# Optimization experiments

Hardware: AMD Instinct MI355X
Metric: run time of the kernel (lower is better)

## Reference

```python
import jax, jax.numpy as jnp
import numpy as np

BINS = 256
SIGMA = 3.0
DELTA = 1.0 / BINS
CENTERS = DELTA * (jnp.arange(BINS, dtype=jnp.float32) + 0.5)  # min=0
W1 = W2 = W3 = 1.0

# --- soft histogram (SoftHistTorch with bins=256, min=0, max=1, sigma=3) ---

def _soft_hist(flat):
    # flat: [N] -> hist: [BINS]
    d = flat[None, :] - CENTERS[:, None]                      # [BINS, N]
    h = jax.nn.sigmoid(SIGMA * (d + DELTA / 2)) - jax.nn.sigmoid(SIGMA * (d - DELTA / 2))
    return h.sum(axis=1)


def _color_uniform(x):
    # x: [B,H,W]; uniform_loss = mean_b sum_bins h*log(h) (only where h>0)
    flat = x.reshape(x.shape[0], -1)
    hist = jax.vmap(_soft_hist)(flat)                          # [B, BINS]
    safe = jnp.where(hist > 0, hist, 1.0)
    hlogh = jnp.where(hist > 0, hist * jnp.log(safe), 0.0)
    return hlogh.sum(axis=1).mean()

# --- SSIM (standard pytorch-ssim: 11x11 gaussian window, sigma=1.5, 1 channel) ---

def _gauss_window(size=11, sigma=1.5):
    c = np.arange(size, dtype=np.float64) - size // 2
    g = np.exp(-(c ** 2) / (2.0 * sigma ** 2))
    g /= g.sum()
    w = np.outer(g, g)
    return jnp.asarray(w, dtype=jnp.float32)[None, None]       # [1,1,11,11]

_WIN = _gauss_window()
_PAD = 11 // 2


def _conv(img):
    return jax.lax.conv_general_dilated(img, _WIN, (1, 1), [(_PAD, _PAD), (_PAD, _PAD)])


def _ssim(img1, img2):
    C1, C2 = 0.01 ** 2, 0.03 ** 2
    mu1, mu2 = _conv(img1), _conv(img2)
    mu1_sq, mu2_sq, mu1_mu2 = mu1 * mu1, mu2 * mu2, mu1 * mu2
    s1 = _conv(img1 * img1) - mu1_sq
    s2 = _conv(img2 * img2) - mu2_sq
    s12 = _conv(img1 * img2) - mu1_mu2
    num = (2 * mu1_mu2 + C1) * (2 * s12 + C2)
    den = (mu1_sq + mu2_sq + C1) * (s1 + s2 + C2)
    return (num / den).mean()


def _norm01(t):
    t = t - t.min()
    return t / t.max()


def setup_inputs() -> dict:
    key = jax.random.key(0)
    k1, k2, k3 = jax.random.split(key, 3)
    x = jax.random.uniform(k1, (8, 1, 384, 384), dtype=jnp.float32)
    target = jax.random.uniform(k2, (8, 384, 384), dtype=jnp.float32)
    depth = jax.random.uniform(k3, (8, 384, 384), dtype=jnp.float32)
    return {"x": x, "target": target, "depth": depth}


def reference(x, target, depth):
    x = jnp.squeeze(x, 1)                 # [B,H,W]
    output = _norm01(x)                   # torch in-place normalization aliases x
    IR = _norm01(target)
    depth_n = _norm01(depth)
    B = x.shape[0]
    uniform_loss = _color_uniform(output)
    depth_loss = jnp.sum(output * depth_n) / B   # x aliases normalized output in torch
    ssim_loss = 1.0 - _ssim(output[:, None], IR[:, None])
    loss = W1 * 1e-06 * uniform_loss + W2 * 1e-05 * depth_loss + W3 * ssim_loss
    return loss
```

## Files before the change

kernel.cpp:

```cpp
#include <hip/hip_runtime.h>
#include <math.h>

#define NTHR 256
#define K_FINE 2048
#define HW 147456
#define N1 1179648
#define IMG 384
#define NHC 24
#define NHIST 192
#define NTILE 1152

#define WS_PMM    0
#define WS_HIST   1536
#define WS_DEPTH  17920
#define WS_SSIM   18112
#define WS_UNIF   19264
#define WS_TICKET 19520

#define HRS (42*33)
#define SMEMF (42*43*2 + 3*HRS)

__global__ __launch_bounds__(NTHR) void k_minmax(
        const float* __restrict__ x, const float* __restrict__ tg,
        const float* __restrict__ dp, float* __restrict__ wsf)
{
    __shared__ float swred[4][8];
    const int tid = threadIdx.x, bid = blockIdx.x;
    const float4* x4 = (const float4*)x  + bid * 1152;
    const float4* t4 = (const float4*)tg + bid * 1152;
    const float4* d4 = (const float4*)dp + bid * 1152;
    float mn0 = 3.4e38f, mx0 = -3.4e38f;
    float mn1 = 3.4e38f, mx1 = -3.4e38f;
    float mn2 = 3.4e38f, mx2 = -3.4e38f;
    for (int i = tid; i < 1152; i += NTHR) {
        float4 v = x4[i];
        mn0 = fminf(mn0, fminf(fminf(v.x, v.y), fminf(v.z, v.w)));
        mx0 = fmaxf(mx0, fmaxf(fmaxf(v.x, v.y), fmaxf(v.z, v.w)));
        v = t4[i];
        mn1 = fminf(mn1, fminf(fminf(v.x, v.y), fminf(v.z, v.w)));
        mx1 = fmaxf(mx1, fmaxf(fmaxf(v.x, v.y), fmaxf(v.z, v.w)));
        v = d4[i];
        mn2 = fminf(mn2, fminf(fminf(v.x, v.y), fminf(v.z, v.w)));
        mx2 = fmaxf(mx2, fmaxf(fmaxf(v.x, v.y), fmaxf(v.z, v.w)));
    }
    #pragma unroll
    for (int off = 32; off; off >>= 1) {
        mn0 = fminf(mn0, __shfl_down(mn0, off, 64));
        mx0 = fmaxf(mx0, __shfl_down(mx0, off, 64));
        mn1 = fminf(mn1, __shfl_down(mn1, off, 64));
        mx1 = fmaxf(mx1, __shfl_down(mx1, off, 64));
        mn2 = fminf(mn2, __shfl_down(mn2, off, 64));
        mx2 = fmaxf(mx2, __shfl_down(mx2, off, 64));
    }
    if ((tid & 63) == 0) {
        int w = tid >> 6;
        swred[w][0] = mn0; swred[w][1] = mx0; swred[w][2] = mn1;
        swred[w][3] = mx1; swred[w][4] = mn2; swred[w][5] = mx2;
    }
    __syncthreads();
    if (tid == 0) {
        #pragma unroll
        for (int w = 1; w < 4; w++) {
            swred[0][0] = fminf(swred[0][0], swred[w][0]);
            swred[0][1] = fmaxf(swred[0][1], swred[w][1]);
            swred[0][2] = fminf(swred[0][2], swred[w][2]);
            swred[0][3] = fmaxf(swred[0][3], swred[w][3]);
            swred[0][4] = fminf(swred[0][4], swred[w][4]);
            swred[0][5] = fmaxf(swred[0][5], swred[w][5]);
        }
        wsf[WS_PMM +        bid * 2]     = swred[0][0];
        wsf[WS_PMM +        bid * 2 + 1] = swred[0][1];
        wsf[WS_PMM + 512  + bid * 2]     = swred[0][2];
        wsf[WS_PMM + 512  + bid * 2 + 1] = swred[0][3];
        wsf[WS_PMM + 1024 + bid * 2]     = swred[0][4];
        wsf[WS_PMM + 1024 + bid * 2 + 1] = swred[0][5];
        if (bid == 0) ((int*)wsf)[WS_TICKET] = 0;
    }
    if (tid < 64) ((int*)wsf)[WS_HIST + bid * 64 + tid] = 0;
}

__device__ __forceinline__ void reduce_minmax(
        const float* __restrict__ wsf, float swred[4][8], int tid,
        float& xmn, float& xinv, float& tmn, float& tinv, float& dmn, float& dinv)
{
    const float2* pm = (const float2*)&wsf[WS_PMM];
    float2 a = pm[tid], b = pm[256 + tid], c = pm[512 + tid];
    float mn0 = a.x, mx0 = a.y, mn1 = b.x, mx1 = b.y, mn2 = c.x, mx2 = c.y;
    #pragma unroll
    for (int off = 32; off; off >>= 1) {
        mn0 = fminf(mn0, __shfl_down(mn0, off, 64));
        mx0 = fmaxf(mx0, __shfl_down(mx0, off, 64));
        mn1 = fminf(mn1, __shfl_down(mn1, off, 64));
        mx1 = fmaxf(mx1, __shfl_down(mx1, off, 64));
        mn2 = fminf(mn2, __shfl_down(mn2, off, 64));
        mx2 = fmaxf(mx2, __shfl_down(mx2, off, 64));
    }
    if ((tid & 63) == 0) {
        int w = tid >> 6;
        swred[w][0] = mn0; swred[w][1] = mx0; swred[w][2] = mn1;
        swred[w][3] = mx1; swred[w][4] = mn2; swred[w][5] = mx2;
    }
    __syncthreads();
    mn0 = fminf(fminf(swred[0][0], swred[1][0]), fminf(swred[2][0], swred[3][0]));
    mx0 = fmaxf(fmaxf(swred[0][1], swred[1][1]), fmaxf(swred[2][1], swred[3][1]));
    mn1 = fminf(fminf(swred[0][2], swred[1][2]), fminf(swred[2][2], swred[3][2]));
    mx1 = fmaxf(fmaxf(swred[0][3], swred[1][3]), fmaxf(swred[2][3], swred[3][3]));
    mn2 = fminf(fminf(swred[0][4], swred[1][4]), fminf(swred[2][4], swred[3][4]));
    mx2 = fmaxf(fmaxf(swred[0][5], swred[1][5]), fmaxf(swred[2][5], swred[3][5]));
    xmn = mn0; xinv = 1.0f / (mx0 - mn0);
    tmn = mn1; tinv = 1.0f / (mx1 - mn1);
    dmn = mn2; dinv = 1.0f / (mx2 - mn2);
    __syncthreads();
}

__global__ __launch_bounds__(NTHR) void k_work(
        const float* __restrict__ x, const float* __restrict__ tg,
        const float* __restrict__ dp, float* __restrict__ wsf)
{
    __shared__ float smem[SMEMF];
    __shared__ float swred[4][8];
    const int tid = threadIdx.x, bid = blockIdx.x;

    float xmn, xinv, tmn, tinv, dmn, dinv;
    reduce_minmax(wsf, swred, tid, xmn, xinv, tmn, tinv, dmn, dinv);

    if (bid < NTILE) {
        float g[11];
        {
            float s = 0.f;
            #pragma unroll
            for (int i = 0; i < 11; i++) {
                float dd = (float)(i - 5);
                g[i] = expf(-dd * dd / 4.5f);
                s += g[i];
            }
            float is = 1.0f / s;
            #pragma unroll
            for (int i = 0; i < 11; i++) g[i] *= is;
        }
        float* sO  = smem;
        float* sI  = smem + 42 * 43;
        float* hr0 = smem + 2 * 42 * 43;
        float* hr1 = hr0 + HRS;
        float* hr2 = hr1 + HRS;
        int img = bid / 144;
        int tl  = bid % 144;
        int ty0 = (tl / 12) * 32 - 5;
        int tx0 = (tl % 12) * 32 - 5;
        const float* xb = x  + (size_t)img * HW;
        const float* tb = tg + (size_t)img * HW;
        for (int idx = tid; idx < 42 * 42; idx += NTHR) {
            int rr = idx / 42, cc = idx % 42;
            int gy = ty0 + rr, gx = tx0 + cc;
            float xv = 0.f, tv = 0.f;
            if (gy >= 0 && gy < IMG && gx >= 0 && gx < IMG) {
                int o = gy * IMG + gx;
                xv = (xb[o] - xmn) * xinv;
                tv = (tb[o] - tmn) * tinv;
            }
            sO[rr * 43 + cc] = xv; sI[rr * 43 + cc] = tv;
        }
        __syncthreads();
        for (int idx = tid; idx < 42 * 32; idx += NTHR) {
            int rr = idx >> 5, cx = idx & 31;
            const float* rowO = sO + rr * 43 + cx;
            const float* rowI = sI + rr * 43 + cx;
            float so = 0, si = 0;
            #pragma unroll
            for (int d = 0; d < 11; d++) { so += g[d] * rowO[d]; si += g[d] * rowI[d]; }
            hr0[rr * 33 + cx] = so; hr1[rr * 33 + cx] = si;
        }
        __syncthreads();
        const int ox = tid & 31, oy0 = (tid >> 5) << 2;
        float mu1[4], mu2[4];
        {
            float w0[14], w1[14];
            #pragma unroll
            for (int k = 0; k < 14; k++) {
                int hb = (oy0 + k) * 33 + ox;
                w0[k] = hr0[hb]; w1[k] = hr1[hb];
            }
            #pragma unroll
            for (int p = 0; p < 4; p++) {
                float m1 = 0, m2 = 0;
                #pragma unroll
                for (int dy = 0; dy < 11; dy++) {
                    m1 += g[dy] * w0[p + dy];
                    m2 += g[dy] * w1[p + dy];
                }
                mu1[p] = m1; mu2[p] = m2;
            }
        }
        __syncthreads();
        for (int idx = tid; idx < 42 * 32; idx += NTHR) {
            int rr = idx >> 5, cx = idx & 31;
            const float* rowO = sO + rr * 43 + cx;
            const float* rowI = sI + rr * 43 + cx;
            float soo = 0, sii = 0, soi = 0;
            #pragma unroll
            for (int d = 0; d < 11; d++) {
                float o = rowO[d], ii = rowI[d], w = g[d];
                soo += w * o * o; sii += w * ii * ii; soi += w * o * ii;
            }
            int hb = rr * 33 + cx;
            hr0[hb] = soo; hr1[hb] = sii; hr2[hb] = soi;
        }
        __syncthreads();
        const float C1 = 1e-4f, C2 = 9e-4f;
        float lsum = 0.f;
        {
            float w0[14], w1[14], w2[14];
            #pragma unroll
            for (int k = 0; k < 14; k++) {
                int hb = (oy0 + k) * 33 + ox;
                w0[k] = hr0[hb]; w1[k] = hr1[hb]; w2[k] = hr2[hb];
            }
            #pragma unroll
            for (int p = 0; p < 4; p++) {
                float m11 = 0, m22 = 0, m12 = 0;
                #pragma unroll
                for (int dy = 0; dy < 11; dy++) {
                    float w = g[dy];
                    m11 += w * w0[p + dy];
                    m22 += w * w1[p + dy];
                    m12 += w * w2[p + dy];
                }
                float mu1s = mu1[p] * mu1[p], mu2s = mu2[p] * mu2[p];
                float mu12 = mu1[p] * mu2[p];
                float s1 = m11 - mu1s, s2 = m22 - mu2s, s12 = m12 - mu12;
                lsum += ((2.f * mu12 + C1) * (2.f * s12 + C2))
                      / ((mu1s + mu2s + C1) * (s1 + s2 + C2));
            }
        }
        #pragma unroll
        for (int off = 32; off; off >>= 1) lsum += __shfl_down(lsum, off, 64);
        if ((tid & 63) == 0) swred[tid >> 6][6] = lsum;
        __syncthreads();
        if (tid == 0)
            wsf[WS_SSIM + bid] = swred[0][6] + swred[1][6] + swred[2][6] + swred[3][6];
    } else {
        int c = bid - NTILE;
        int* lh = (int*)smem;
        for (int i = tid; i < K_FINE; i += NTHR) lh[i] = 0;
        __syncthreads();
        int batch = c / NHC, chunk = c % NHC;
        const float4* x4 = (const float4*)x  + (size_t)batch * (HW / 4) + chunk * 1536;
        const float4* d4 = (const float4*)dp + (size_t)batch * (HW / 4) + chunk * 1536;
        float dsum = 0.f;
        for (int i = tid; i < 1536; i += NTHR) {
            float4 xv = x4[i], dv = d4[i];
            float o0 = (xv.x - xmn) * xinv, o1 = (xv.y - xmn) * xinv;
            float o2 = (xv.z - xmn) * xinv, o3 = (xv.w - xmn) * xinv;
            dsum += o0 * ((dv.x - dmn) * dinv) + o1 * ((dv.y - dmn) * dinv)
                  + o2 * ((dv.z - dmn) * dinv) + o3 * ((dv.w - dmn) * dinv);
            int j0 = min(K_FINE - 1, max(0, (int)(o0 * K_FINE)));
            int j1 = min(K_FINE - 1, max(0, (int)(o1 * K_FINE)));
            int j2 = min(K_FINE - 1, max(0, (int)(o2 * K_FINE)));
            int j3 = min(K_FINE - 1, max(0, (int)(o3 * K_FINE)));
            atomicAdd(lh + j0, 1); atomicAdd(lh + j1, 1);
            atomicAdd(lh + j2, 1); atomicAdd(lh + j3, 1);
        }
        __syncthreads();
        int* gh = (int*)wsf + WS_HIST + batch * K_FINE;
        for (int i = tid; i < K_FINE; i += NTHR) {
            int v = lh[i];
            if (v) atomicAdd(gh + i, v);
        }
        #pragma unroll
        for (int off = 32; off; off >>= 1) dsum += __shfl_down(dsum, off, 64);
        if ((tid & 63) == 0) swred[tid >> 6][6] = dsum;
        __syncthreads();
        if (tid == 0)
            wsf[WS_DEPTH + c] = swred[0][6] + swred[1][6] + swred[2][6] + swred[3][6];
    }
}

__global__ __launch_bounds__(NTHR) void k_soft_final(
        float* __restrict__ wsf, float* __restrict__ out)
{
    __shared__ int lh[K_FINE];
    __shared__ float s8[8];
    __shared__ int amLast;
    const int tid = threadIdx.x, bid = blockIdx.x;
    int batch = bid >> 5;
    const int* gh = (const int*)wsf + WS_HIST + batch * K_FINE;
    for (int i = tid; i < K_FINE; i += NTHR) lh[i] = gh[i];
    __syncthreads();
    int binLocal = tid >> 5, slice = tid & 31;
    int bin = (bid & 31) * 8 + binLocal;
    const float delta = 1.0f / 256.0f;
    const float r   = expf(3.0f * delta);
    const float rm1 = r - 1.0f;
    const float c32 = expf(-3.0f * 32.0f / (float)K_FINE);
    float L = (float)bin * delta;
    float u = expf(3.0f * (L - ((float)slice + 0.5f) * (1.0f / (float)K_FINE)));
    float h = 0.f;
    #pragma unroll 4
    for (int j = slice; j < K_FINE; j += 32) {
        float cnt = (float)lh[j];
        float t1 = 1.0f + u;
        float t2 = fmaf(u, r, 1.0f);
        h = fmaf(cnt * (u * rm1), __builtin_amdgcn_rcpf(t1 * t2), h);
        u *= c32;
    }
    #pragma unroll
    for (int off = 16; off; off >>= 1) h += __shfl_down(h, off, 32);
    if (slice == 0) s8[binLocal] = h;
    __syncthreads();
    if (tid == 0) {
        float hl = 0.f;
        #pragma unroll
        for (int b = 0; b < 8; b++) {
            float hh = s8[b];
            hl += (hh > 0.f) ? hh * logf(hh) : 0.f;
        }
        wsf[WS_UNIF + bid] = hl;
        __threadfence();
        int old = atomicAdd((int*)wsf + WS_TICKET, 1);
        amLast = (old == 255);
    }
    __syncthreads();
    if (amLast) {
        __threadfence();
        float a = 0.f, bsum = 0.f, c = 0.f;
        for (int i = tid; i < NHIST; i += NTHR) a    += wsf[WS_DEPTH + i];
        for (int i = tid; i < NTILE; i += NTHR) bsum += wsf[WS_SSIM + i];
        for (int i = tid; i < 256;   i += NTHR) c    += wsf[WS_UNIF + i];
        float* ra = (float*)lh; float* rb = ra + 256; float* rc = rb + 256;
        ra[tid] = a; rb[tid] = bsum; rc[tid] = c;
        __syncthreads();
        for (int s = 128; s; s >>= 1) {
            if (tid < s) {
                ra[tid] += ra[tid + s];
                rb[tid] += rb[tid + s];
                rc[tid] += rc[tid + s];
            }
            __syncthreads();
        }
        if (tid == 0) {
            float uniform  = rc[0] / 8.0f;
            float depthL   = ra[0] / 8.0f;
            float ssimMean = rb[0] / (float)N1;
            out[0] = 1e-6f * uniform + 1e-5f * depthL + (1.0f - ssimMean);
        }
    }
}

extern "C" void kernel_launch(void* const* d_in, const int* in_sizes, int n_in,
                              void* d_out, int out_size, void* d_ws, size_t ws_size,
                              hipStream_t stream) {
    const float* x  = (const float*)d_in[0];
    const float* tg = (const float*)d_in[1];
    const float* dp = (const float*)d_in[2];
    float* wsf = (float*)d_ws;
    float* out = (float*)d_out;
    hipLaunchKernelGGL(k_minmax,     dim3(256),          dim3(NTHR), 0, stream, x, tg, dp, wsf);
    hipLaunchKernelGGL(k_work,       dim3(NTILE+NHIST),  dim3(NTHR), 0, stream, x, tg, dp, wsf);
    hipLaunchKernelGGL(k_soft_final, dim3(256),          dim3(NTHR), 0, stream, wsf, out);
}
```

Before: 40.62 us.

## Compute depth loss algebraically from raw sums in minmax pass

The depth term sum(norm(x)*norm(d)) is expanded algebraically into raw sums Σxd, Σx and Σd, which are accumulated in the first min/max pass while the data is already loaded. The final reduction reconstructs the normalized product from these sums and the global min/inv-range. The histogram blocks in the work kernel no longer read the depth tensor, and they are regrouped into fewer, larger chunks. This removes a second full read of depth but risks float cancellation error in the expanded formula, since Σxd and the correction terms are large and close in magnitude.

```diff
diff --git a/kernel.cpp b/kernel.cpp
--- a/kernel.cpp
+++ b/kernel.cpp
@@ -6,16 +6,18 @@
 #define HW 147456
 #define N1 1179648
 #define IMG 384
-#define NHC 24
-#define NHIST 192
+#define NHC 16
+#define NCHUNK 128
 #define NTILE 1152
-
-#define WS_PMM    0
-#define WS_HIST   1536
-#define WS_DEPTH  17920
-#define WS_SSIM   18112
-#define WS_UNIF   19264
-#define WS_TICKET 19520
+#define TOTAL (NTILE + NCHUNK)
+#define NSOFT 256
+
+#define WS_PMM  0
+#define WS_SUM  1536
+#define WS_CTR  2304
+#define WS_HIST 2312
+#define WS_SSIM (WS_HIST + 8*K_FINE)
+#define WS_UNIF (WS_SSIM + NTILE)
 
 #define HRS (42*33)
 #define SMEMF (42*43*2 + 3*HRS)
@@ -24,7 +26,7 @@
         const float* __restrict__ x, const float* __restrict__ tg,
         const float* __restrict__ dp, float* __restrict__ wsf)
 {
-    __shared__ float swred[4][8];
+    __shared__ float swred[4][12];
     const int tid = threadIdx.x, bid = blockIdx.x;
     const float4* x4 = (const float4*)x  + bid * 1152;
     const float4* t4 = (const float4*)tg + bid * 1152;
@@ -32,16 +34,18 @@
     float mn0 = 3.4e38f, mx0 = -3.4e38f;
     float mn1 = 3.4e38f, mx1 = -3.4e38f;
     float mn2 = 3.4e38f, mx2 = -3.4e38f;
+    float sx = 0.f, sd = 0.f, sxd = 0.f;
     for (int i = tid; i < 1152; i += NTHR) {
-        float4 v = x4[i];
-        mn0 = fminf(mn0, fminf(fminf(v.x, v.y), fminf(v.z, v.w)));
-        mx0 = fmaxf(mx0, fmaxf(fmaxf(v.x, v.y), fmaxf(v.z, v.w)));
-        v = t4[i];
-        mn1 = fminf(mn1, fminf(fminf(v.x, v.y), fminf(v.z, v.w)));
-        mx1 = fmaxf(mx1, fmaxf(fmaxf(v.x, v.y), fmaxf(v.z, v.w)));
-        v = d4[i];
-        mn2 = fminf(mn2, fminf(fminf(v.x, v.y), fminf(v.z, v.w)));
-        mx2 = fmaxf(mx2, fmaxf(fmaxf(v.x, v.y), fmaxf(v.z, v.w)));
+        float4 a = x4[i], b = t4[i], d = d4[i];
+        mn0 = fminf(mn0, fminf(fminf(a.x, a.y), fminf(a.z, a.w)));
+        mx0 = fmaxf(mx0, fmaxf(fmaxf(a.x, a.y), fmaxf(a.z, a.w)));
+        mn1 = fminf(mn1, fminf(fminf(b.x, b.y), fminf(b.z, b.w)));
+        mx1 = fmaxf(mx1, fmaxf(fmaxf(b.x, b.y), fmaxf(b.z, b.w)));
+        mn2 = fminf(mn2, fminf(fminf(d.x, d.y), fminf(d.z, d.w)));
+        mx2 = fmaxf(mx2, fmaxf(fmaxf(d.x, d.y), fmaxf(d.z, d.w)));
+        sx += (a.x + a.y) + (a.z + a.w);
+        sd += (d.x + d.y) + (d.z + d.w);
+        sxd = fmaf(a.x, d.x, fmaf(a.y, d.y, fmaf(a.z, d.z, fmaf(a.w, d.w, sxd))));
     }
     #pragma unroll
     for (int off = 32; off; off >>= 1) {
@@ -51,11 +55,15 @@
         mx1 = fmaxf(mx1, __shfl_down(mx1, off, 64));
         mn2 = fminf(mn2, __shfl_down(mn2, off, 64));
         mx2 = fmaxf(mx2, __shfl_down(mx2, off, 64));
+        sx  += __shfl_down(sx,  off, 64);
+        sd  += __shfl_down(sd,  off, 64);
+        sxd += __shfl_down(sxd, off, 64);
     }
     if ((tid & 63) == 0) {
         int w = tid >> 6;
         swred[w][0] = mn0; swred[w][1] = mx0; swred[w][2] = mn1;
         swred[w][3] = mx1; swred[w][4] = mn2; swred[w][5] = mx2;
+        swred[w][6] = sxd; swred[w][7] = sx;  swred[w][8] = sd;
     }
     __syncthreads();
     if (tid == 0) {
@@ -67,6 +75,9 @@
             swred[0][3] = fmaxf(swred[0][3], swred[w][3]);
             swred[0][4] = fminf(swred[0][4], swred[w][4]);
             swred[0][5] = fmaxf(swred[0][5], swred[w][5]);
+            swred[0][6] += swred[w][6];
+            swred[0][7] += swred[w][7];
+            swred[0][8] += swred[w][8];
         }
         wsf[WS_PMM +        bid * 2]     = swred[0][0];
         wsf[WS_PMM +        bid * 2 + 1] = swred[0][1];
@@ -74,13 +85,16 @@
         wsf[WS_PMM + 512  + bid * 2 + 1] = swred[0][3];
         wsf[WS_PMM + 1024 + bid * 2]     = swred[0][4];
         wsf[WS_PMM + 1024 + bid * 2 + 1] = swred[0][5];
-        if (bid == 0) ((int*)wsf)[WS_TICKET] = 0;
+        wsf[WS_SUM +        bid] = swred[0][6];
+        wsf[WS_SUM + 256  + bid] = swred[0][7];
+        wsf[WS_SUM + 512  + bid] = swred[0][8];
+        if (bid == 0) ((int*)wsf)[WS_CTR] = 0;
     }
     if (tid < 64) ((int*)wsf)[WS_HIST + bid * 64 + tid] = 0;
 }
 
 __device__ __forceinline__ void reduce_minmax(
-        const float* __restrict__ wsf, float swred[4][8], int tid,
+        const float* __restrict__ wsf, float swred[4][12], int tid,
         float& xmn, float& xinv, float& tmn, float& tinv, float& dmn, float& dinv)
 {
     const float2* pm = (const float2*)&wsf[WS_PMM];
@@ -115,14 +129,15 @@
 
 __global__ __launch_bounds__(NTHR) void k_work(
         const float* __restrict__ x, const float* __restrict__ tg,
-        const float* __restrict__ dp, float* __restrict__ wsf)
+        float* __restrict__ wsf)
 {
     __shared__ float smem[SMEMF];
-    __shared__ float swred[4][8];
+    __shared__ float swred[4][12];
     const int tid = threadIdx.x, bid = blockIdx.x;
 
     float xmn, xinv, tmn, tinv, dmn, dinv;
     reduce_minmax(wsf, swred, tid, xmn, xinv, tmn, tinv, dmn, dinv);
+    (void)dmn; (void)dinv;
 
     if (bid < NTILE) {
         float g[11];
@@ -243,16 +258,12 @@
         int* lh = (int*)smem;
         for (int i = tid; i < K_FINE; i += NTHR) lh[i] = 0;
         __syncthreads();
-        int batch = c / NHC, chunk = c % NHC;
-        const float4* x4 = (const float4*)x  + (size_t)batch * (HW / 4) + chunk * 1536;
-        const float4* d4 = (const float4*)dp + (size_t)batch * (HW / 4) + chunk * 1536;
-        float dsum = 0.f;
-        for (int i = tid; i < 1536; i += NTHR) {
-            float4 xv = x4[i], dv = d4[i];
+        int batch = c >> 4, chunk = c & 15;
+        const float4* x4 = (const float4*)x + (size_t)batch * (HW / 4) + chunk * 2304;
+        for (int i = tid; i < 2304; i += NTHR) {
+            float4 xv = x4[i];
             float o0 = (xv.x - xmn) * xinv, o1 = (xv.y - xmn) * xinv;
             float o2 = (xv.z - xmn) * xinv, o3 = (xv.w - xmn) * xinv;
-            dsum += o0 * ((dv.x - dmn) * dinv) + o1 * ((dv.y - dmn) * dinv)
-                  + o2 * ((dv.z - dmn) * dinv) + o3 * ((dv.w - dmn) * dinv);
             int j0 = min(K_FINE - 1, max(0, (int)(o0 * K_FINE)));
             int j1 = min(K_FINE - 1, max(0, (int)(o1 * K_FINE)));
             int j2 = min(K_FINE - 1, max(0, (int)(o2 * K_FINE)));
@@ -266,12 +277,6 @@
             int v = lh[i];
             if (v) atomicAdd(gh + i, v);
         }
-        #pragma unroll
-        for (int off = 32; off; off >>= 1) dsum += __shfl_down(dsum, off, 64);
-        if ((tid & 63) == 0) swred[tid >> 6][6] = dsum;
-        __syncthreads();
-        if (tid == 0)
-            wsf[WS_DEPTH + c] = swred[0][6] + swred[1][6] + swred[2][6] + swred[3][6];
     }
 }
 
@@ -279,6 +284,7 @@
         float* __restrict__ wsf, float* __restrict__ out)
 {
     __shared__ int lh[K_FINE];
+    __shared__ float swred[4][12];
     __shared__ float s8[8];
     __shared__ int amLast;
     const int tid = threadIdx.x, bid = blockIdx.x;
@@ -316,33 +322,42 @@
         }
         wsf[WS_UNIF + bid] = hl;
         __threadfence();
-        int old = atomicAdd((int*)wsf + WS_TICKET, 1);
-        amLast = (old == 255);
-    }
-    __syncthreads();
-    if (amLast) {
-        __threadfence();
-        float a = 0.f, bsum = 0.f, c = 0.f;
-        for (int i = tid; i < NHIST; i += NTHR) a    += wsf[WS_DEPTH + i];
-        for (int i = tid; i < NTILE; i += NTHR) bsum += wsf[WS_SSIM + i];
-        for (int i = tid; i < 256;   i += NTHR) c    += wsf[WS_UNIF + i];
-        float* ra = (float*)lh; float* rb = ra + 256; float* rc = rb + 256;
-        ra[tid] = a; rb[tid] = bsum; rc[tid] = c;
-        __syncthreads();
-        for (int s = 128; s; s >>= 1) {
-            if (tid < s) {
-                ra[tid] += ra[tid + s];
-                rb[tid] += rb[tid + s];
-                rc[tid] += rc[tid + s];
-            }
-            __syncthreads();
-        }
-        if (tid == 0) {
-            float uniform  = rc[0] / 8.0f;
-            float depthL   = ra[0] / 8.0f;
-            float ssimMean = rb[0] / (float)N1;
-            out[0] = 1e-6f * uniform + 1e-5f * depthL + (1.0f - ssimMean);
-        }
+        int old = atomicAdd((int*)wsf + WS_CTR, 1);
+        amLast = (old == NSOFT - 1);
+    }
+    __syncthreads();
+    if (!amLast) return;
+
+    __threadfence();
+    float xmn, xinv, tmn, tinv, dmn, dinv;
+    reduce_minmax(wsf, swred, tid, xmn, xinv, tmn, tinv, dmn, dinv);
+    (void)tmn; (void)tinv;
+    float sxd  = wsf[WS_SUM + tid];
+    float sx   = wsf[WS_SUM + 256 + tid];
+    float sd   = wsf[WS_SUM + 512 + tid];
+    float bsum = 0.f;
+    for (int i = tid; i < NTILE; i += NTHR) bsum += wsf[WS_SSIM + i];
+    float c = wsf[WS_UNIF + tid];
+    float* r0 = (float*)lh;
+    float* r1 = r0 + 256; float* r2 = r1 + 256;
+    float* r3 = r2 + 256; float* r4 = r3 + 256;
+    r0[tid] = sxd; r1[tid] = sx; r2[tid] = sd; r3[tid] = bsum; r4[tid] = c;
+    __syncthreads();
+    for (int s = 128; s; s >>= 1) {
+        if (tid < s) {
+            r0[tid] += r0[tid + s]; r1[tid] += r1[tid + s];
+            r2[tid] += r2[tid + s]; r3[tid] += r3[tid + s];
+            r4[tid] += r4[tid + s];
+        }
+        __syncthreads();
+    }
+    if (tid == 0) {
+        float SXD = r0[0], SX = r1[0], SD = r2[0];
+        float uniform  = r4[0] / 8.0f;
+        float depthNum = SXD - xmn * SD - dmn * SX + (float)N1 * xmn * dmn;
+        float depthL   = xinv * dinv * depthNum / 8.0f;
+        float ssimMean = r3[0] / (float)N1;
+        out[0] = 1e-6f * uniform + 1e-5f * depthL + (1.0f - ssimMean);
     }
 }
 
@@ -354,7 +369,7 @@
     const float* dp = (const float*)d_in[2];
     float* wsf = (float*)d_ws;
     float* out = (float*)d_out;
-    hipLaunchKernelGGL(k_minmax,     dim3(256),          dim3(NTHR), 0, stream, x, tg, dp, wsf);
-    hipLaunchKernelGGL(k_work,       dim3(NTILE+NHIST),  dim3(NTHR), 0, stream, x, tg, dp, wsf);
-    hipLaunchKernelGGL(k_soft_final, dim3(256),          dim3(NTHR), 0, stream, wsf, out);
-}
+    hipLaunchKernelGGL(k_minmax,     dim3(256),   dim3(NTHR), 0, stream, x, tg, dp, wsf);
+    hipLaunchKernelGGL(k_work,       dim3(TOTAL), dim3(NTHR), 0, stream, x, tg, wsf);
+    hipLaunchKernelGGL(k_soft_final, dim3(NSOFT), dim3(NTHR), 0, stream, wsf, out);
+}
```

Result: faster. 39.74 us (-2.2%).
